# Kernel optimization log

Hardware: AMD Instinct MI355X
Metric: run time of the kernel (lower is better)

Reference implementation:

```python
import jax, jax.numpy as jnp
import numpy as np

D_MODEL = 1024
NUM_HEADS = 16
D_K = D_MODEL // NUM_HEADS
NEG = -1000000000.0


def setup_inputs() -> dict:
    key = jax.random.key(0)
    ks = jax.random.split(key, 9)
    B, S, D = 2, 2048, D_MODEL
    scale = 1.0 / np.sqrt(D)
    return {
        "query": jax.random.normal(ks[0], (B, S, D), jnp.float32),
        "key": jax.random.normal(ks[1], (B, S, D), jnp.float32),
        "value": jax.random.normal(ks[2], (B, S, D), jnp.float32),
        "mask": jax.random.randint(ks[3], (B, S, S), 0, 2, jnp.int32),
        # torch nn.Linear stores weight as (out_features, in_features); y = x @ W.T
        "W_q": jax.random.normal(ks[4], (D, D), jnp.float32) * scale,
        "W_k": jax.random.normal(ks[5], (D, D), jnp.float32) * scale,
        "W_v": jax.random.normal(ks[6], (D, D), jnp.float32) * scale,
        "W_o": jax.random.normal(ks[7], (D, D), jnp.float32) * scale,
        "b_o": jax.random.normal(ks[8], (D,), jnp.float32) * 0.01,
    }


def reference(query, key, value, mask, W_q, W_k, W_v, W_o, b_o):
    B, S, D = query.shape
    H, dk = NUM_HEADS, D_K
    # projections (torch Linear: x @ W.T), then split heads -> [B, H, S, dk]
    def split_heads(x, W):
        return jnp.einsum('bsd,ed->bse', x, W).reshape(B, S, H, dk).transpose(0, 2, 1, 3)
    Q = split_heads(query, W_q)
    K = split_heads(key, W_k)
    V = split_heads(value, W_v)
    scores = jnp.einsum('bhqd,bhkd->bhqk', Q, K) / jnp.sqrt(jnp.float32(dk))
    scores = jnp.where(mask[:, None, :, :] == 0, NEG, scores)
    attn = jax.nn.softmax(scores, axis=-1)  # dropout inactive in eval mode
    out = jnp.einsum('bhqk,bhkd->bhqd', attn, V)  # [B, H, S, dk]
    out = out.transpose(0, 2, 1, 3).reshape(B, S, D)
    return jnp.einsum('bsd,ed->bse', out, W_o) + b_o
```

## Files before the change

kernel.cpp:

```cpp
#include <hip/hip_runtime.h>
#include <hip/hip_bf16.h>
#include <stdint.h>

typedef __attribute__((ext_vector_type(4))) float f32x4;
typedef __attribute__((ext_vector_type(8))) short bf16x8;
typedef __attribute__((ext_vector_type(4))) unsigned short us4;
typedef unsigned short ushort_t;
typedef unsigned long long u64;

#define LOG2E 1.44269504088896340f
#define NEGB  -1.0e9f

__device__ __forceinline__ unsigned short f2bf(float x){
  union { float f; uint32_t u; } v; v.f = x;
  uint32_t u = v.u + 0x7fffu + ((v.u >> 16) & 1u);
  return (unsigned short)(u >> 16);
}

__device__ __forceinline__ void gld16(const void* g, void* l){
  __builtin_amdgcn_global_load_lds(
      (const __attribute__((address_space(1))) unsigned int*)g,
      (__attribute__((address_space(3))) unsigned int*)l, 16, 0, 0);
}

__global__ void prep_all(const float4* __restrict__ q, const float4* __restrict__ k,
                         const float4* __restrict__ v, const float4* __restrict__ wq,
                         const float4* __restrict__ wk, const float4* __restrict__ wv,
                         const float4* __restrict__ wo, ushort_t* __restrict__ dst){
  int i = blockIdx.x * 256 + threadIdx.x;
  const float4* src; int base;
  if      (i < 1048576){ src = q;  base = 0; }
  else if (i < 2097152){ src = k;  base = 1048576; }
  else if (i < 3145728){ src = v;  base = 2097152; }
  else if (i < 3407872){ src = wq; base = 3145728; }
  else if (i < 3670016){ src = wk; base = 3407872; }
  else if (i < 3932160){ src = wv; base = 3670016; }
  else                 { src = wo; base = 3932160; }
  float4 f = src[i - base];
  us4 o; o.x = f2bf(f.x); o.y = f2bf(f.y); o.z = f2bf(f.z); o.w = f2bf(f.w);
  ((us4*)dst)[i] = o;
}

__global__ void gemm_qkv(const ushort_t* __restrict__ qb, const ushort_t* __restrict__ kb,
                         const ushort_t* __restrict__ vb, const ushort_t* __restrict__ wqb,
                         const ushort_t* __restrict__ wkb, const ushort_t* __restrict__ wvb,
                         ushort_t* __restrict__ Qh, ushort_t* __restrict__ Kh,
                         ushort_t* __restrict__ Vt, float qscale,
                         const int4* __restrict__ mask, u64* __restrict__ mb){
  __shared__ ushort_t smem[16384];
#define AsQ(c) (smem + (c)*4096)
#define BsQ(c) (smem + 8192 + (c)*4096)
  const int z = blockIdx.z;
  if (z == 3){
    int bid2 = blockIdx.x + (blockIdx.y << 5);
    #pragma unroll
    for (int rep = 0; rep < 2; rep++){
      int w = bid2 * 512 + rep * 256 + threadIdx.x;
      const int4* p = mask + (size_t)w * 16;
      u64 bits = 0;
      #pragma unroll
      for (int j = 0; j < 16; j++){
        int4 m = p[j];
        bits |= (u64)(m.x != 0) << (j*4);
        bits |= (u64)(m.y != 0) << (j*4+1);
        bits |= (u64)(m.z != 0) << (j*4+2);
        bits |= (u64)(m.w != 0) << (j*4+3);
      }
      mb[w] = bits;
    }
    return;
  }
  const ushort_t* A = (z == 0) ? qb  : (z == 1) ? kb  : vb;
  const ushort_t* B = (z == 0) ? wqb : (z == 1) ? wkb : wvb;
  ushort_t*       C = (z == 0) ? Qh  : (z == 1) ? Kh  : Vt;
  const float scale = (z == 0) ? qscale : 1.0f;

  const int tid = threadIdx.x, wave = tid >> 6, lane = tid & 63;
  const int l15 = lane & 15;
  const int m0 = blockIdx.x * 128, n0 = blockIdx.y * 128;
  const int wr = wave >> 1, wc = wave & 1;
  f32x4 acc[4][4] = {};

  const ushort_t* Ag = A + (size_t)(m0 + wave*16 + (lane>>2)) * 1024 + (lane&3)*8;
  const ushort_t* Bg = B + (size_t)(n0 + wave*16 + (lane>>2)) * 1024 + (lane&3)*8;

#define GSTAGE(k0, c) do { \
    gld16(Ag + (k0),         AsQ(c) + wave*512); \
    gld16(Ag + 65536 + (k0), AsQ(c) + (4+wave)*512); \
    gld16(Bg + (k0),         BsQ(c) + wave*512); \
    gld16(Bg + 65536 + (k0), BsQ(c) + (4+wave)*512); } while(0)

  GSTAGE(0, 0);
  int cur = 0;
  for (int k0 = 0; k0 < 1024; k0 += 32){
    __syncthreads();
    if (k0 < 992) GSTAGE(k0 + 32, cur ^ 1);
    bf16x8 a[4], b[4];
    #pragma unroll
    for (int i = 0; i < 4; i++){
      a[i] = *(const bf16x8*)&AsQ(cur)[(wr*64 + i*16 + l15)*32 + (lane>>4)*8];
      b[i] = *(const bf16x8*)&BsQ(cur)[(wc*64 + i*16 + l15)*32 + (lane>>4)*8];
    }
    __builtin_amdgcn_s_setprio(1);
    #pragma unroll
    for (int i = 0; i < 4; i++)
      #pragma unroll
      for (int j = 0; j < 4; j++)
        acc[i][j] = __builtin_amdgcn_mfma_f32_16x16x32_bf16(a[i], b[j], acc[i][j], 0, 0, 0);
    __builtin_amdgcn_s_setprio(0);
    cur ^= 1;
  }

  if (z < 2){
    #pragma unroll
    for (int i = 0; i < 4; i++){
      #pragma unroll
      for (int j = 0; j < 4; j++){
        #pragma unroll
        for (int r = 0; r < 4; r++){
          int row = m0 + wr*64 + i*16 + (lane>>4)*4 + r;
          int col = n0 + wc*64 + j*16 + l15;
          int bb = row >> 11, s = row & 2047, h = col >> 6, d = col & 63;
          C[((size_t)(bb*16 + h)*2048 + s)*64 + d] = f2bf(acc[i][j][r] * scale);
        }
      }
    }
  } else {
    ushort_t* T = smem;
    #pragma unroll
    for (int hh = 0; hh < 2; hh++){
      __syncthreads();
      if (wc == hh){
        #pragma unroll
        for (int i = 0; i < 4; i++){
          #pragma unroll
          for (int j = 0; j < 4; j++){
            int n = j*16 + l15;
            int mb2 = wr*64 + i*16 + (lane>>4)*4;
            us4 pk;
            pk.x = f2bf(acc[i][j][0]); pk.y = f2bf(acc[i][j][1]);
            pk.z = f2bf(acc[i][j][2]); pk.w = f2bf(acc[i][j][3]);
            *(us4*)&T[n*136 + mb2] = pk;
          }
        }
      }
      __syncthreads();
      #pragma unroll
      for (int cc = 0; cc < 4; cc++){
        int chunk = cc*256 + tid;
        int n = chunk >> 4, mc = chunk & 15;
        uint4 val = *(uint4*)&T[n*136 + mc*8];
        int col = n0 + hh*64 + n;
        int hcol = col >> 6, d = col & 63;
        int row = m0 + mc*8;
        int bb2 = row >> 11, s = row & 2047;
        *(uint4*)&C[((size_t)(bb2*16 + hcol)*64 + d)*2048 + s] = val;
      }
    }
  }
}

__global__ __launch_bounds__(512)
void gemm_out(const ushort_t* __restrict__ A, const ushort_t* __restrict__ B,
              float* __restrict__ C, const float* __restrict__ bias){
  __shared__ ushort_t As[2][4096];
  __shared__ ushort_t Bs[2][4096];
  const int tid = threadIdx.x, wave = tid >> 6, lane = tid & 63;
  const int l15 = lane & 15;
  const int m0 = blockIdx.x * 128, n0 = blockIdx.y * 128;
  const int wr = wave >> 1, wc = wave & 1;
  f32x4 acc[2][4] = {};

  const ushort_t* Ag = A + (size_t)(m0 + wave*16 + (lane>>2)) * 1024 + (lane&3)*8;
  const ushort_t* Bg = B + (size_t)(n0 + wave*16 + (lane>>2)) * 1024 + (lane&3)*8;

#define GSTAGE2(k0, c) do { \
    gld16(Ag + (k0), &As[c][wave*512]); \
    gld16(Bg + (k0), &Bs[c][wave*512]); } while(0)

  GSTAGE2(0, 0);
  int cur = 0;
  for (int k0 = 0; k0 < 1024; k0 += 32){
    __syncthreads();
    if (k0 < 992) GSTAGE2(k0 + 32, cur ^ 1);
    bf16x8 a[2], b[4];
    #pragma unroll
    for (int i = 0; i < 2; i++)
      a[i] = *(const bf16x8*)&As[cur][(wr*32 + i*16 + l15)*32 + (lane>>4)*8];
    #pragma unroll
    for (int j = 0; j < 4; j++)
      b[j] = *(const bf16x8*)&Bs[cur][(wc*64 + j*16 + l15)*32 + (lane>>4)*8];
    __builtin_amdgcn_s_setprio(1);
    #pragma unroll
    for (int i = 0; i < 2; i++)
      #pragma unroll
      for (int j = 0; j < 4; j++)
        acc[i][j] = __builtin_amdgcn_mfma_f32_16x16x32_bf16(a[i], b[j], acc[i][j], 0, 0, 0);
    __builtin_amdgcn_s_setprio(0);
    cur ^= 1;
  }

  #pragma unroll
  for (int i = 0; i < 2; i++){
    #pragma unroll
    for (int j = 0; j < 4; j++){
      #pragma unroll
      for (int r = 0; r < 4; r++){
        int row = m0 + wr*32 + i*16 + (lane>>4)*4 + r;
        int col = n0 + wc*64 + j*16 + l15;
        C[(size_t)row * 1024 + col] = acc[i][j][r] + bias[col];
      }
    }
  }
}

__global__ void attn_fused(const ushort_t* __restrict__ Qh, const ushort_t* __restrict__ Kh,
                           const ushort_t* __restrict__ Vt, const u64* __restrict__ MB,
                           ushort_t* __restrict__ AO){
  __shared__ ushort_t Ks[3][4096];
  __shared__ ushort_t Vs[3][4096];
  __shared__ ushort_t Pb[8][1024];

  const int tid = threadIdx.x, wave = tid >> 6, lane = tid & 63;
  const int g = lane >> 4, l15 = lane & 15;
  const int wg = ((blockIdx.x & 7) << 6) | (blockIdx.x >> 3);
  const int qt = wg & 15, h = (wg >> 4) & 15, b = wg >> 8;
  const int q0 = qt * 128;

  const ushort_t* Qb = Qh + ((size_t)(b*16 + h)*2048 + q0) * 64;
  const ushort_t* Kb = Kh + ((size_t)(b*16 + h)*2048) * 64;
  const ushort_t* Vb = Vt + ((size_t)(b*16 + h)*64) * 2048;
  const u64* wp = MB + ((size_t)b*2048 + q0 + wave*16 + l15) * 32;

  bf16x8 qf[2];
  #pragma unroll
  for (int ks = 0; ks < 2; ks++)
    qf[ks] = *(const bf16x8*)&Qb[(wave*16 + l15)*64 + ks*32 + g*8];

  bf16x8 onesb;
  #pragma unroll
  for (int j = 0; j < 8; j++) onesb[j] = (short)0x3F80;

  f32x4 o[4] = {};
  f32x4 osum = {};

  const int srow = lane >> 3;
  const int scol = ((lane & 7) * 16) ^ (srow << 4);
  const ushort_t* Kg = Kb + (size_t)(wave*8 + srow)*64   + (scol >> 1);
  const ushort_t* Vg = Vb + (size_t)(wave*8 + srow)*2048 + (scol >> 1);
  ushort_t* pb = &Pb[wave][0];
  const int xv = (l15 & 7) << 4;
  const int g4 = g * 4;

  int kaddr[4][2], vaddr[4][2], pwb[4], prb[2];
  #pragma unroll
  for (int nf = 0; nf < 4; nf++){
    int row = nf*16 + l15;
    #pragma unroll
    for (int ks = 0; ks < 2; ks++){
      int cb = (ks*64 + g*16) ^ ((row & 7) << 4);
      kaddr[nf][ks] = row*64 + (cb >> 1);
    }
  }
  #pragma unroll
  for (int df = 0; df < 4; df++){
    int vrow = df*16 + l15;
    #pragma unroll
    for (int c = 0; c < 2; c++){
      int cb = (c*64 + g*16) ^ ((vrow & 7) << 4);
      vaddr[df][c] = vrow*64 + (cb >> 1);
    }
  }
  #pragma unroll
  for (int nf = 0; nf < 4; nf++)
    pwb[nf] = l15*128 + ((nf*32 + g*8) ^ xv);
  #pragma unroll
  for (int c = 0; c < 2; c++)
    prb[c] = l15*128 + ((c*64 + g*16) ^ xv);

#define ASTAGE(t, c) do { \
    gld16(Kg + (size_t)(t)*4096, &Ks[c][wave*512]); \
    gld16(Vg + (t)*64,           &Vs[c][wave*512]); } while(0)

  ASTAGE(0, 0);
  u64 w = wp[0];
  bf16x8 pa[2];
  int qc = 0;
  int pc = 2;

  for (int t = 0; t < 32; t++){
    __syncthreads();
    int sc = (qc + 1 == 3) ? 0 : qc + 1;
    if (t < 31) ASTAGE(t + 1, sc);
    u64 wnext = (t < 31) ? wp[t + 1] : 0;

    f32x4 sa[4] = {};
    __builtin_amdgcn_s_setprio(1);
    #pragma unroll
    for (int nf = 0; nf < 4; nf++){
      #pragma unroll
      for (int ks = 0; ks < 2; ks++){
        bf16x8 kf = *(const bf16x8*)&Ks[qc][kaddr[nf][ks]];
        sa[nf] = __builtin_amdgcn_mfma_f32_16x16x32_bf16(kf, qf[ks], sa[nf], 0, 0, 0);
      }
    }
    if (t > 0){
      #pragma unroll
      for (int df = 0; df < 4; df++){
        #pragma unroll
        for (int c = 0; c < 2; c++){
          bf16x8 vf = *(const bf16x8*)&Vs[pc][vaddr[df][c]];
          o[df] = __builtin_amdgcn_mfma_f32_16x16x32_bf16(pa[c], vf, o[df], 0, 0, 0);
        }
      }
      osum = __builtin_amdgcn_mfma_f32_16x16x32_bf16(pa[0], onesb, osum, 0, 0, 0);
      osum = __builtin_amdgcn_mfma_f32_16x16x32_bf16(pa[1], onesb, osum, 0, 0, 0);
    }
    __builtin_amdgcn_s_setprio(0);

    uint32_t s0 = ((uint32_t)w) >> g4;
    uint32_t s1 = ((uint32_t)(w >> 32)) >> g4;
    float p[4][4];
    #pragma unroll
    for (int nf = 0; nf < 4; nf++){
      uint32_t ws = (nf < 2) ? s0 : s1;
      const int sh = (nf & 1) * 16;
      #pragma unroll
      for (int r = 0; r < 4; r++){
        float s = ((ws >> (sh + r)) & 1u) ? sa[nf][r] : NEGB;
        p[nf][r] = __builtin_amdgcn_exp2f(s);
      }
    }

    #pragma unroll
    for (int nf = 0; nf < 4; nf++){
      __hip_bfloat162 lo, hi;
      lo.x = __float2bfloat16(p[nf][0]); lo.y = __float2bfloat16(p[nf][1]);
      hi.x = __float2bfloat16(p[nf][2]); hi.y = __float2bfloat16(p[nf][3]);
      uint2 pk; pk.x = *(uint32_t*)&lo; pk.y = *(uint32_t*)&hi;
      *(uint2*)((char*)pb + pwb[nf]) = pk;
    }
    asm volatile("s_waitcnt lgkmcnt(0)" ::: "memory");
    #pragma unroll
    for (int c = 0; c < 2; c++)
      pa[c] = *(const bf16x8*)((const char*)pb + prb[c]);

    w = wnext;
    pc = qc; qc = sc;
  }

  __builtin_amdgcn_s_setprio(1);
  #pragma unroll
  for (int df = 0; df < 4; df++){
    #pragma unroll
    for (int c = 0; c < 2; c++){
      bf16x8 vf = *(const bf16x8*)&Vs[pc][vaddr[df][c]];
      o[df] = __builtin_amdgcn_mfma_f32_16x16x32_bf16(pa[c], vf, o[df], 0, 0, 0);
    }
  }
  osum = __builtin_amdgcn_mfma_f32_16x16x32_bf16(pa[0], onesb, osum, 0, 0, 0);
  osum = __builtin_amdgcn_mfma_f32_16x16x32_bf16(pa[1], onesb, osum, 0, 0, 0);
  __builtin_amdgcn_s_setprio(0);

  float li[4];
  #pragma unroll
  for (int r = 0; r < 4; r++) li[r] = 1.0f / osum[r];
  #pragma unroll
  for (int df = 0; df < 4; df++){
    #pragma unroll
    for (int r = 0; r < 4; r++){
      int s = q0 + wave*16 + g4 + r;
      int d = h*64 + df*16 + l15;
      AO[((size_t)b*2048 + s)*1024 + d] = f2bf(o[df][r] * li[r]);
    }
  }
}

extern "C" void kernel_launch(void* const* d_in, const int* in_sizes, int n_in,
                              void* d_out, int out_size, void* d_ws, size_t ws_size,
                              hipStream_t stream){
  const float* q   = (const float*)d_in[0];
  const float* k   = (const float*)d_in[1];
  const float* v   = (const float*)d_in[2];
  const int*   msk = (const int*)  d_in[3];
  const float* wq  = (const float*)d_in[4];
  const float* wk  = (const float*)d_in[5];
  const float* wv  = (const float*)d_in[6];
  const float* wo  = (const float*)d_in[7];
  const float* bo  = (const float*)d_in[8];

  char* ws = (char*)d_ws;
  ushort_t* conv = (ushort_t*)ws;
  ushort_t* qb  = conv;
  ushort_t* kb  = conv + 4194304;
  ushort_t* vb  = conv + 8388608;
  ushort_t* wqb = conv + 12582912;
  ushort_t* wkb = conv + 13631488;
  ushort_t* wvb = conv + 14680064;
  ushort_t* wob = conv + 15728640;
  u64*      mbits = (u64*)(ws + 33554432);
  ushort_t* Qh  = (ushort_t*)(ws + 34603008);
  ushort_t* Kh  = (ushort_t*)(ws + 42991616);
  ushort_t* Vt  = (ushort_t*)d_out;
  ushort_t* AO  = qb;

  prep_all<<<16384, 256, 0, stream>>>((const float4*)q, (const float4*)k,
      (const float4*)v, (const float4*)wq, (const float4*)wk, (const float4*)wv,
      (const float4*)wo, conv);

  const float qscale = 0.125f * LOG2E;
  gemm_qkv<<<dim3(32, 8, 4), 256, 0, stream>>>(qb, kb, vb, wqb, wkb, wvb,
                                               Qh, Kh, Vt, qscale,
                                               (const int4*)msk, mbits);

  attn_fused<<<512, 512, 0, stream>>>(Qh, Kh, Vt, mbits, AO);

  gemm_out<<<dim3(32, 8), 512, 0, stream>>>(AO, wob, (float*)d_out, bo);
}
```

Baseline: 128.7 us.

## Fuse fp32-to-bf16 activation conversion into QKV GEMM A-tile loads

The separate conversion pass for the query, key and value activations is removed. The QKV GEMM now streams fp32 A tiles into LDS with an XOR-swizzled layout and converts them to bf16 while building MFMA fragments, and only the weights are still pre-converted. This drops a full write and read of the bf16 activation copies, about 48MB of traffic, but doubles A-tile global and LDS bytes per stage, raises LDS use to 48KB, and adds conversion ALU work inside the main loop.

```diff
diff --git a/kernel.cpp b/kernel.cpp
--- a/kernel.cpp
+++ b/kernel.cpp
@@ -17,39 +17,42 @@
   return (unsigned short)(u >> 16);
 }
 
+__device__ __forceinline__ uint32_t pkbf(float a, float b){
+  __hip_bfloat162 t;
+  t.x = __float2bfloat16(a); t.y = __float2bfloat16(b);
+  union { __hip_bfloat162 h; uint32_t u; } c; c.h = t;
+  return c.u;
+}
+
 __device__ __forceinline__ void gld16(const void* g, void* l){
   __builtin_amdgcn_global_load_lds(
       (const __attribute__((address_space(1))) unsigned int*)g,
       (__attribute__((address_space(3))) unsigned int*)l, 16, 0, 0);
 }
 
-__global__ void prep_all(const float4* __restrict__ q, const float4* __restrict__ k,
-                         const float4* __restrict__ v, const float4* __restrict__ wq,
-                         const float4* __restrict__ wk, const float4* __restrict__ wv,
-                         const float4* __restrict__ wo, ushort_t* __restrict__ dst){
+__global__ void prep_w(const float4* __restrict__ wq, const float4* __restrict__ wk,
+                       const float4* __restrict__ wv, const float4* __restrict__ wo,
+                       ushort_t* __restrict__ dst){
   int i = blockIdx.x * 256 + threadIdx.x;
   const float4* src; int base;
-  if      (i < 1048576){ src = q;  base = 0; }
-  else if (i < 2097152){ src = k;  base = 1048576; }
-  else if (i < 3145728){ src = v;  base = 2097152; }
-  else if (i < 3407872){ src = wq; base = 3145728; }
-  else if (i < 3670016){ src = wk; base = 3407872; }
-  else if (i < 3932160){ src = wv; base = 3670016; }
-  else                 { src = wo; base = 3932160; }
+  if      (i < 262144){ src = wq; base = 0; }
+  else if (i < 524288){ src = wk; base = 262144; }
+  else if (i < 786432){ src = wv; base = 524288; }
+  else                { src = wo; base = 786432; }
   float4 f = src[i - base];
   us4 o; o.x = f2bf(f.x); o.y = f2bf(f.y); o.z = f2bf(f.z); o.w = f2bf(f.w);
-  ((us4*)dst)[i] = o;
-}
-
-__global__ void gemm_qkv(const ushort_t* __restrict__ qb, const ushort_t* __restrict__ kb,
-                         const ushort_t* __restrict__ vb, const ushort_t* __restrict__ wqb,
+  ((us4*)dst)[3145728 + i] = o;
+}
+
+__global__ void gemm_qkv(const float* __restrict__ qf32, const float* __restrict__ kf32,
+                         const float* __restrict__ vf32, const ushort_t* __restrict__ wqb,
                          const ushort_t* __restrict__ wkb, const ushort_t* __restrict__ wvb,
                          ushort_t* __restrict__ Qh, ushort_t* __restrict__ Kh,
                          ushort_t* __restrict__ Vt, float qscale,
                          const int4* __restrict__ mask, u64* __restrict__ mb){
-  __shared__ ushort_t smem[16384];
-#define AsQ(c) (smem + (c)*4096)
-#define BsQ(c) (smem + 8192 + (c)*4096)
+  __shared__ char smemc[49152];
+#define AsQ(c) (smemc + (c)*16384)
+#define BsQ(c) ((ushort_t*)(smemc + 32768 + (c)*8192))
   const int z = blockIdx.z;
   if (z == 3){
     int bid2 = blockIdx.x + (blockIdx.y << 5);
@@ -70,9 +73,9 @@
     }
     return;
   }
-  const ushort_t* A = (z == 0) ? qb  : (z == 1) ? kb  : vb;
-  const ushort_t* B = (z == 0) ? wqb : (z == 1) ? wkb : wvb;
-  ushort_t*       C = (z == 0) ? Qh  : (z == 1) ? Kh  : Vt;
+  const float*    A = (z == 0) ? qf32 : (z == 1) ? kf32 : vf32;
+  const ushort_t* B = (z == 0) ? wqb  : (z == 1) ? wkb  : wvb;
+  ushort_t*       C = (z == 0) ? Qh   : (z == 1) ? Kh   : Vt;
   const float scale = (z == 0) ? qscale : 1.0f;
 
   const int tid = threadIdx.x, wave = tid >> 6, lane = tid & 63;
@@ -81,14 +84,17 @@
   const int wr = wave >> 1, wc = wave & 1;
   f32x4 acc[4][4] = {};
 
-  const ushort_t* Ag = A + (size_t)(m0 + wave*16 + (lane>>2)) * 1024 + (lane&3)*8;
+  const float* Agw = A + (size_t)(m0 + wave*32 + (lane>>3)) * 1024
+                       + (((lane&7) ^ (lane>>3)) << 2);
   const ushort_t* Bg = B + (size_t)(n0 + wave*16 + (lane>>2)) * 1024 + (lane&3)*8;
 
 #define GSTAGE(k0, c) do { \
-    gld16(Ag + (k0),         AsQ(c) + wave*512); \
-    gld16(Ag + 65536 + (k0), AsQ(c) + (4+wave)*512); \
-    gld16(Bg + (k0),         BsQ(c) + wave*512); \
-    gld16(Bg + 65536 + (k0), BsQ(c) + (4+wave)*512); } while(0)
+    gld16(Agw + (k0),         AsQ(c) + wave*4096); \
+    gld16(Agw + 8192  + (k0), AsQ(c) + wave*4096 + 1024); \
+    gld16(Agw + 16384 + (k0), AsQ(c) + wave*4096 + 2048); \
+    gld16(Agw + 24576 + (k0), AsQ(c) + wave*4096 + 3072); \
+    gld16(Bg + (k0),          BsQ(c) + wave*512); \
+    gld16(Bg + 65536 + (k0),  BsQ(c) + (4+wave)*512); } while(0)
 
   GSTAGE(0, 0);
   int cur = 0;
@@ -96,10 +102,18 @@
     __syncthreads();
     if (k0 < 992) GSTAGE(k0 + 32, cur ^ 1);
     bf16x8 a[4], b[4];
+    const int g2 = lane >> 4;
     #pragma unroll
     for (int i = 0; i < 4; i++){
-      a[i] = *(const bf16x8*)&AsQ(cur)[(wr*64 + i*16 + l15)*32 + (lane>>4)*8];
-      b[i] = *(const bf16x8*)&BsQ(cur)[(wc*64 + i*16 + l15)*32 + (lane>>4)*8];
+      int r = wr*64 + i*16 + l15;
+      const char* rowp = AsQ(cur) + r*128;
+      float4 f0 = *(const float4*)(rowp + ((((g2<<1)    ) ^ (r & 7)) << 4));
+      float4 f1 = *(const float4*)(rowp + ((((g2<<1) + 1) ^ (r & 7)) << 4));
+      union { uint4 u; bf16x8 v; } cv;
+      cv.u.x = pkbf(f0.x, f0.y); cv.u.y = pkbf(f0.z, f0.w);
+      cv.u.z = pkbf(f1.x, f1.y); cv.u.w = pkbf(f1.z, f1.w);
+      a[i] = cv.v;
+      b[i] = *(const bf16x8*)&BsQ(cur)[(wc*64 + i*16 + l15)*32 + g2*8];
     }
     __builtin_amdgcn_s_setprio(1);
     #pragma unroll
@@ -126,7 +140,7 @@
       }
     }
   } else {
-    ushort_t* T = smem;
+    ushort_t* T = (ushort_t*)smemc;
     #pragma unroll
     for (int hh = 0; hh < 2; hh++){
       __syncthreads();
@@ -391,9 +405,6 @@
 
   char* ws = (char*)d_ws;
   ushort_t* conv = (ushort_t*)ws;
-  ushort_t* qb  = conv;
-  ushort_t* kb  = conv + 4194304;
-  ushort_t* vb  = conv + 8388608;
   ushort_t* wqb = conv + 12582912;
   ushort_t* wkb = conv + 13631488;
   ushort_t* wvb = conv + 14680064;
@@ -402,14 +413,13 @@
   ushort_t* Qh  = (ushort_t*)(ws + 34603008);
   ushort_t* Kh  = (ushort_t*)(ws + 42991616);
   ushort_t* Vt  = (ushort_t*)d_out;
-  ushort_t* AO  = qb;
-
-  prep_all<<<16384, 256, 0, stream>>>((const float4*)q, (const float4*)k,
-      (const float4*)v, (const float4*)wq, (const float4*)wk, (const float4*)wv,
-      (const float4*)wo, conv);
+  ushort_t* AO  = conv;
+
+  prep_w<<<4096, 256, 0, stream>>>((const float4*)wq, (const float4*)wk,
+                                   (const float4*)wv, (const float4*)wo, conv);
 
   const float qscale = 0.125f * LOG2E;
-  gemm_qkv<<<dim3(32, 8, 4), 256, 0, stream>>>(qb, kb, vb, wqb, wkb, wvb,
+  gemm_qkv<<<dim3(32, 8, 4), 256, 0, stream>>>(q, k, v, wqb, wkb, wvb,
                                                Qh, Kh, Vt, qscale,
                                                (const int4*)msk, mbits);
 
```

Result: no change. 130.7 us (+1.5%).
